# Kernel optimization log

Measured on AMD Instinct MI355X. Metric: run time of the kernel, lower is better.

Reference implementation:

```python
import jax, jax.numpy as jnp
import numpy as np
import math

B, S, D, H, PD = 2, 2048, 1024, 16, 3
DK = D // H          # 64
SP = S // H          # 128, required so physics_scores matches scores shape


def setup_inputs() -> dict:
    key = jax.random.key(0)
    ks = jax.random.split(key, 16)
    sc = 0.02
    return {
        "query": jax.random.normal(ks[0], (B, S, D), jnp.float32),
        "key_in": jax.random.normal(ks[1], (B, S, D), jnp.float32),
        "value": jax.random.normal(ks[2], (B, S, D), jnp.float32),
        "physics_info": jax.random.normal(ks[3], (B, SP, PD), jnp.float32),
        "Wq": jax.random.normal(ks[4], (D, D), jnp.float32) * sc,
        "bq": jnp.zeros((D,), jnp.float32),
        "Wk": jax.random.normal(ks[5], (D, D), jnp.float32) * sc,
        "bk": jnp.zeros((D,), jnp.float32),
        "Wv": jax.random.normal(ks[6], (D, D), jnp.float32) * sc,
        "bv": jnp.zeros((D,), jnp.float32),
        "Wo": jax.random.normal(ks[7], (D, D), jnp.float32) * sc,
        "bo": jnp.zeros((D,), jnp.float32),
        "Pw": jax.random.normal(ks[8], (PD, D), jnp.float32),   # physics_weight
        "pb": jnp.zeros((1,), jnp.float32),                      # physics_bias
    }


def reference(query, key_in, value, physics_info, Wq, bq, Wk, bk, Wv, bv, Wo, bo, Pw, pb):
    b, s, d = query.shape
    inv = 1.0 / math.sqrt(DK)
    # project and split heads -> [B, H, S, DK]
    Q = (query @ Wq + bq).reshape(b, s, H, DK).transpose(0, 2, 1, 3)
    K = (key_in @ Wk + bk).reshape(b, s, H, DK).transpose(0, 2, 1, 3)
    V = (value @ Wv + bv).reshape(b, s, H, DK).transpose(0, 2, 1, 3)
    scores = jnp.einsum('bhqd,bhkd->bhqk', Q, K) * inv  # [B,H,S,S]
    # physics constraint: [B,SP,D] -> (expand over heads is a no-op) -> [B,SP*H,DK]
    pc = (physics_info @ Pw).reshape(b, SP * H, DK)
    physics_scores = jnp.einsum('bhqd,bkd->bhqk', Q, pc) * inv  # [B,H,S,S]
    scores = scores + pb[0] * physics_scores
    attn = jax.nn.softmax(scores, axis=-1)  # dropout in eval mode (identity)
    ctx = jnp.einsum('bhqk,bhkd->bhqd', attn, V)
    ctx = ctx.transpose(0, 2, 1, 3).reshape(b, s, d)
    return ctx @ Wo + bo
```

## Files before the change

kernel.cpp:

```cpp
#include <hip/hip_runtime.h>
#include <hip/hip_bf16.h>
#include <stdint.h>
#include <math.h>

typedef __bf16 bf16_t;
typedef __attribute__((ext_vector_type(8))) __bf16 bf16x8;
typedef __attribute__((ext_vector_type(4))) __bf16 bf16x4;
typedef __attribute__((ext_vector_type(4))) short short4_t;
typedef __attribute__((ext_vector_type(4))) float f32x4;

#define GLOBAL_AS(p) ((const __attribute__((address_space(1))) void*)(p))
#define LDS_AS(p)    ((__attribute__((address_space(3))) void*)(p))

#define B_ 2
#define S_ 2048
#define D_ 1024
#define H_ 16
#define DK_ 64
#define SP_ 128

#define QSCALE 0.1803368801111144f

static __device__ inline float fast_exp2(float x) {
#if __has_builtin(__builtin_amdgcn_exp2f)
    return __builtin_amdgcn_exp2f(x);
#else
    return __expf(x * 0.6931471805599453f);
#endif
}

static __device__ inline f32x4 mfma16x16x16bf16(short4_t a, short4_t b, f32x4 c) {
#if __has_builtin(__builtin_amdgcn_mfma_f32_16x16x16bf16_1k)
    return __builtin_amdgcn_mfma_f32_16x16x16bf16_1k(a, b, c, 0, 0, 0);
#else
    asm volatile("v_mfma_f32_16x16x16_bf16 %0, %1, %2, %0" : "+v"(c) : "v"(a), "v"(b));
    return c;
#endif
}

struct WPtrs { const float* w[4]; bf16_t* o[4]; };

__global__ __launch_bounds__(256) void prep(
    const float* __restrict__ q, const float* __restrict__ k,
    const float* __restrict__ v,
    bf16_t* __restrict__ qo, bf16_t* __restrict__ ko, bf16_t* __restrict__ vo,
    WPtrs wp, const float* __restrict__ phys, const float* __restrict__ Pw,
    float* __restrict__ PP) {
    __shared__ bf16_t t[32][33];
    int tid = threadIdx.x;
    for (int bx = blockIdx.x; bx < 11264; bx += 2048) {
        if (bx < 6144) {
            int z = bx >> 11, blk = bx & 2047;
            const float* in = (z == 0) ? q : (z == 1) ? k : v;
            bf16_t* out = (z == 0) ? qo : (z == 1) ? ko : vo;
            size_t i = ((size_t)blk * 256 + tid) * 8;
            f32x4 a = *(const f32x4*)(in + i);
            f32x4 b = *(const f32x4*)(in + i + 4);
            bf16x8 o;
#pragma unroll
            for (int e = 0; e < 4; ++e) { o[e] = (bf16_t)a[e]; o[4 + e] = (bf16_t)b[e]; }
            *(bf16x8*)(out + i) = o;
        } else if (bx < 10240) {
            __syncthreads();
            int idx = bx - 6144;
            int z = idx >> 10;
            const float* W = wp.w[z];
            bf16_t* Wt = wp.o[z];
            int gx = (idx & 31) * 32, gy = ((idx >> 5) & 31) * 32;
            int x = tid & 31, y0 = tid >> 5;
#pragma unroll
            for (int j = 0; j < 32; j += 8)
                t[y0 + j][x] = (bf16_t)W[(size_t)(gy + y0 + j) * D_ + gx + x];
            __syncthreads();
#pragma unroll
            for (int j = 0; j < 32; j += 8)
                Wt[(size_t)(gx + y0 + j) * D_ + gy + x] = t[x][y0 + j];
        } else {
            int i = (bx - 10240) * 256 + tid;
            int n = i & (D_ - 1);
            int sb = i >> 10;
            float acc = 0.f;
#pragma unroll
            for (int p = 0; p < 3; ++p)
                acc += phys[sb * 3 + p] * Pw[p * D_ + n];
            PP[i] = acc;
        }
    }
}

#define TSTR 272

__global__ __launch_bounds__(256) void qkv_gemm(
    const bf16_t* __restrict__ Qi, const bf16_t* __restrict__ Ki,
    const bf16_t* __restrict__ Vi,
    const bf16_t* __restrict__ WqT, const bf16_t* __restrict__ WkT,
    const bf16_t* __restrict__ WvT,
    const float* __restrict__ bq, const float* __restrict__ bk,
    const float* __restrict__ bv,
    bf16_t* __restrict__ Qo, bf16_t* __restrict__ Ko, bf16_t* __restrict__ Vo,
    const float* __restrict__ PP, const float* __restrict__ pbp) {
    __shared__ alignas(16) char smem[40960];
    bf16_t* lA = (bf16_t*)smem;
    bf16_t* lB = (bf16_t*)(smem + 16384);
    int z = blockIdx.z;
    const bf16_t* A = (z == 0) ? Qi : (z == 1) ? Ki : Vi;
    const bf16_t* Bt = (z == 0) ? WqT : (z == 1) ? WkT : WvT;
    const float* bias = (z == 0) ? bq : (z == 1) ? bk : bv;

    int tid = threadIdx.x;
    int lane = tid & 63, wid = tid >> 6;
    int quad = lane >> 4, l15 = lane & 15;
    int bm = blockIdx.x * 128;
    int bn = blockIdx.y * 128;
    int wm = (wid >> 1) * 64, wn = (wid & 1) * 64;
    f32x4 acc[4][4] = {};

    for (int k0 = 0; k0 < D_; k0 += 64) {
        __syncthreads();
        const char* gA = (const char*)(A + (size_t)bm * D_ + k0);
        const char* gB = (const char*)(Bt + (size_t)bn * D_ + k0);
#pragma unroll
        for (int j = 0; j < 4; ++j) {
            int woff = j * 4096 + wid * 1024;
            int fl = woff + lane * 16;
            int row = fl >> 7, col = fl & 127;
            __builtin_amdgcn_global_load_lds(GLOBAL_AS(gA + (size_t)row * (D_ * 2) + col),
                                             LDS_AS((char*)lA + woff), 16, 0, 0);
            __builtin_amdgcn_global_load_lds(GLOBAL_AS(gB + (size_t)row * (D_ * 2) + col),
                                             LDS_AS((char*)lB + woff), 16, 0, 0);
        }
        __syncthreads();
#pragma unroll
        for (int ks = 0; ks < 2; ++ks) {
            bf16x8 af[4], bfr[4];
#pragma unroll
            for (int i = 0; i < 4; ++i) {
                af[i] = *(const bf16x8*)((const char*)lA + (wm + i * 16 + l15) * 128 + ks * 64 + quad * 16);
                bfr[i] = *(const bf16x8*)((const char*)lB + (wn + i * 16 + l15) * 128 + ks * 64 + quad * 16);
            }
#pragma unroll
            for (int i = 0; i < 4; ++i)
#pragma unroll
                for (int j = 0; j < 4; ++j)
                    acc[i][j] = __builtin_amdgcn_mfma_f32_16x16x32_bf16(af[i], bfr[j], acc[i][j], 0, 0, 0);
        }
    }

    __syncthreads();
    float pb0 = (z == 1) ? pbp[0] : 0.f;
    char* T = smem;
#pragma unroll
    for (int i = 0; i < 4; ++i)
#pragma unroll
        for (int j = 0; j < 4; ++j) {
            int rl0 = wm + i * 16 + quad * 4;
            int c = wn + j * 16 + l15;
            float bv_ = bias[bn + c];
            if (z == 2) {
                bf16x4 t4;
#pragma unroll
                for (int reg = 0; reg < 4; ++reg) t4[reg] = (bf16_t)(acc[i][j][reg] + bv_);
                *(bf16x4*)(T + c * TSTR + rl0 * 2) = t4;
            } else if (z == 1) {
#pragma unroll
                for (int reg = 0; reg < 4; ++reg) {
                    int r = bm + rl0 + reg;
                    int b = r >> 11, s = r & (S_ - 1);
                    float v = acc[i][j][reg] + bv_ +
                              pb0 * PP[((size_t)(b * SP_ + (s >> 4)) << 10) + ((s & 15) << 6) + ((bn + c) & 63)];
                    *(bf16_t*)(T + (rl0 + reg) * TSTR + c * 2) = (bf16_t)v;
                }
            } else {
#pragma unroll
                for (int reg = 0; reg < 4; ++reg)
                    *(bf16_t*)(T + (rl0 + reg) * TSTR + c * 2) = (bf16_t)((acc[i][j][reg] + bv_) * QSCALE);
            }
        }
    __syncthreads();
    if (z == 2) {
        int b = bm >> 11, s0 = bm & (S_ - 1);
        char* gout = (char*)Vo + (((size_t)(b << 10) + bn) * S_ + s0) * 2;
#pragma unroll
        for (int it = 0; it < 8; ++it) {
            int chunk = it * 256 + tid;
            int row = chunk >> 4, c16 = chunk & 15;
            bf16x8 v = *(const bf16x8*)(T + row * TSTR + c16 * 16);
            *(bf16x8*)(gout + (size_t)row * (S_ * 2) + c16 * 16) = v;
        }
    } else {
        bf16_t* O = (z == 0) ? Qo : Ko;
        char* gout = (char*)(O + (size_t)bm * D_ + bn);
#pragma unroll
        for (int it = 0; it < 8; ++it) {
            int chunk = it * 256 + tid;
            int row = chunk >> 4, c16 = chunk & 15;
            bf16x8 v = *(const bf16x8*)(T + row * TSTR + c16 * 16);
            *(bf16x8*)(gout + (size_t)row * (D_ * 2) + c16 * 16) = v;
        }
    }
}

#define KSTR 144
#define VSTR 272

__global__ __launch_bounds__(256) void flash_attn(const bf16_t* Qb,
                                                  const bf16_t* __restrict__ Kb,
                                                  const bf16_t* __restrict__ Vt,
                                                  bf16_t* Ctx) {
    __shared__ alignas(16) char lK[128 * KSTR];
    __shared__ alignas(16) char lV[64 * VSTR];
    int tid = threadIdx.x, lane = tid & 63, wid = tid >> 6;
    int quad = lane >> 4, l15 = lane & 15;
    int q0 = blockIdx.x * 128;
    int h = blockIdx.y, b = blockIdx.z;
    const bf16_t* Qh = Qb + ((size_t)b * S_) * D_ + h * DK_;
    const bf16_t* Kh = Kb + ((size_t)b * S_) * D_ + h * DK_;
    const bf16_t* Vh = Vt + ((size_t)b * D_ + h * DK_) * S_;

    {
        const char* g = (const char*)(Qh + (size_t)q0 * D_);
#pragma unroll
        for (int j = 0; j < 4; ++j) {
            int flat = j * 4096 + tid * 16;
            bf16x8 v = *(const bf16x8*)(g + (size_t)(flat >> 7) * (D_ * 2) + (flat & 127));
            *(bf16x8*)(lK + (flat >> 7) * KSTR + (flat & 127)) = v;
        }
    }
    __syncthreads();
    bf16x8 qf[2][2];
#pragma unroll
    for (int mt = 0; mt < 2; ++mt)
#pragma unroll
        for (int ks = 0; ks < 2; ++ks)
            qf[mt][ks] = *(const bf16x8*)(lK + (wid * 32 + mt * 16 + l15) * KSTR + ks * 64 + quad * 16);

    f32x4 ot[4][2] = {};
    float l_i[2] = {0.f, 0.f};

    for (int t = 0; t < S_ / 128; ++t) {
        const char* gK = (const char*)(Kh + (size_t)t * 128 * D_);
        const char* gV = (const char*)(Vh + (size_t)t * 128);
        bf16x8 vk[4], vv[4];
#pragma unroll
        for (int j = 0; j < 4; ++j) {
            int flat = j * 4096 + tid * 16;
            vk[j] = *(const bf16x8*)(gK + (size_t)(flat >> 7) * (D_ * 2) + (flat & 127));
            vv[j] = *(const bf16x8*)(gV + (size_t)(flat >> 8) * (S_ * 2) + (flat & 255));
        }
        __syncthreads();
#pragma unroll
        for (int j = 0; j < 4; ++j) {
            int flat = j * 4096 + tid * 16;
            *(bf16x8*)(lK + (flat >> 7) * KSTR + (flat & 127)) = vk[j];
            *(bf16x8*)(lV + (flat >> 8) * VSTR + (flat & 255)) = vv[j];
        }
        __syncthreads();

        f32x4 sc[8][2];
#pragma unroll
        for (int kt = 0; kt < 8; ++kt)
#pragma unroll
            for (int mt = 0; mt < 2; ++mt) sc[kt][mt] = (f32x4){0.f, 0.f, 0.f, 0.f};
#pragma unroll
        for (int kt = 0; kt < 8; ++kt) {
            bf16x8 kf0 = *(const bf16x8*)(lK + (kt * 16 + l15) * KSTR + quad * 16);
            bf16x8 kf1 = *(const bf16x8*)(lK + (kt * 16 + l15) * KSTR + 64 + quad * 16);
#pragma unroll
            for (int mt = 0; mt < 2; ++mt) {
                sc[kt][mt] = __builtin_amdgcn_mfma_f32_16x16x32_bf16(kf0, qf[mt][0], sc[kt][mt], 0, 0, 0);
                sc[kt][mt] = __builtin_amdgcn_mfma_f32_16x16x32_bf16(kf1, qf[mt][1], sc[kt][mt], 0, 0, 0);
            }
        }

#pragma unroll
        for (int mt = 0; mt < 2; ++mt) {
            float rsum = 0.f;
#pragma unroll
            for (int kt = 0; kt < 8; ++kt)
#pragma unroll
                for (int r = 0; r < 4; ++r) {
                    float p = fast_exp2(sc[kt][mt][r]);
                    sc[kt][mt][r] = p;
                    rsum += p;
                }
            rsum += __shfl_xor(rsum, 16, 64);
            rsum += __shfl_xor(rsum, 32, 64);
            l_i[mt] += rsum;
        }

#pragma unroll
        for (int kt = 0; kt < 8; ++kt) {
            short4_t bp[2];
#pragma unroll
            for (int mt = 0; mt < 2; ++mt) {
                bf16x4 t4;
#pragma unroll
                for (int r = 0; r < 4; ++r) t4[r] = (bf16_t)sc[kt][mt][r];
                bp[mt] = *(short4_t*)&t4;
            }
#pragma unroll
            for (int dt = 0; dt < 4; ++dt) {
                bf16x4 a4 = *(const bf16x4*)(lV + (dt * 16 + l15) * VSTR + kt * 32 + quad * 8);
                short4_t ap = *(short4_t*)&a4;
#pragma unroll
                for (int mt = 0; mt < 2; ++mt)
                    ot[dt][mt] = mfma16x16x16bf16(ap, bp[mt], ot[dt][mt]);
            }
        }
    }

    __syncthreads();
#pragma unroll
    for (int mt = 0; mt < 2; ++mt) {
        float inv_l = 1.0f / l_i[mt];
#pragma unroll
        for (int dt = 0; dt < 4; ++dt) {
            bf16x4 t4;
#pragma unroll
            for (int r = 0; r < 4; ++r) t4[r] = (bf16_t)(ot[dt][mt][r] * inv_l);
            *(bf16x4*)(lK + (wid * 32 + mt * 16 + l15) * KSTR + dt * 32 + quad * 8) = t4;
        }
    }
    __syncthreads();
    {
        char* gout = (char*)(Ctx + ((size_t)b * S_ + q0) * D_ + h * DK_);
#pragma unroll
        for (int j = 0; j < 4; ++j) {
            int flat = j * 4096 + tid * 16;
            bf16x8 v = *(const bf16x8*)(lK + (flat >> 7) * KSTR + (flat & 127));
            *(bf16x8*)(gout + (size_t)(flat >> 7) * (D_ * 2) + (flat & 127)) = v;
        }
    }
}

__global__ __launch_bounds__(256) void gemm_out(const bf16_t* __restrict__ A,
                                                const bf16_t* __restrict__ Bt,
                                                const float* __restrict__ bias,
                                                float* __restrict__ C) {
    __shared__ alignas(16) bf16_t lA[64 * 64];
    __shared__ alignas(16) bf16_t lB[128 * 64];
    int tid = threadIdx.x;
    int lane = tid & 63, wid = tid >> 6;
    int quad = lane >> 4, l15 = lane & 15;
    int bm = blockIdx.x * 64;
    int bn = blockIdx.y * 128;
    int wm = (wid >> 1) * 32, wn = (wid & 1) * 64;
    f32x4 acc[2][4] = {};

    for (int k0 = 0; k0 < D_; k0 += 64) {
        __syncthreads();
        const char* gA = (const char*)(A + (size_t)bm * D_ + k0);
        const char* gB = (const char*)(Bt + (size_t)bn * D_ + k0);
#pragma unroll
        for (int j = 0; j < 2; ++j) {
            int fl = j * 4096 + tid * 16;
            int row = fl >> 7, col = fl & 127;
            __builtin_amdgcn_global_load_lds(GLOBAL_AS(gA + (size_t)row * (D_ * 2) + col),
                                             LDS_AS((char*)lA + fl), 16, 0, 0);
        }
#pragma unroll
        for (int j = 0; j < 4; ++j) {
            int fl = j * 4096 + tid * 16;
            int row = fl >> 7, col = fl & 127;
            __builtin_amdgcn_global_load_lds(GLOBAL_AS(gB + (size_t)row * (D_ * 2) + col),
                                             LDS_AS((char*)lB + fl), 16, 0, 0);
        }
        __syncthreads();
#pragma unroll
        for (int ks = 0; ks < 2; ++ks) {
            bf16x8 af[2], bfr[4];
#pragma unroll
            for (int i = 0; i < 2; ++i)
                af[i] = *(const bf16x8*)((const char*)lA + (wm + i * 16 + l15) * 128 + ks * 64 + quad * 16);
#pragma unroll
            for (int j = 0; j < 4; ++j)
                bfr[j] = *(const bf16x8*)((const char*)lB + (wn + j * 16 + l15) * 128 + ks * 64 + quad * 16);
#pragma unroll
            for (int i = 0; i < 2; ++i)
#pragma unroll
                for (int j = 0; j < 4; ++j)
                    acc[i][j] = __builtin_amdgcn_mfma_f32_16x16x32_bf16(af[i], bfr[j], acc[i][j], 0, 0, 0);
        }
    }
#pragma unroll
    for (int i = 0; i < 2; ++i)
#pragma unroll
        for (int j = 0; j < 4; ++j) {
            int r0 = bm + wm + i * 16 + quad * 4;
            int c = bn + wn + j * 16 + l15;
            float bv_ = bias[c];
#pragma unroll
            for (int reg = 0; reg < 4; ++reg)
                C[(size_t)(r0 + reg) * D_ + c] = acc[i][j][reg] + bv_;
        }
}

extern "C" void kernel_launch(void* const* d_in, const int* in_sizes, int n_in,
                              void* d_out, int out_size, void* d_ws, size_t ws_size,
                              hipStream_t stream) {
    const float* query  = (const float*)d_in[0];
    const float* key_in = (const float*)d_in[1];
    const float* value  = (const float*)d_in[2];
    const float* phys   = (const float*)d_in[3];
    const float* Wq     = (const float*)d_in[4];
    const float* bq     = (const float*)d_in[5];
    const float* Wk     = (const float*)d_in[6];
    const float* bk     = (const float*)d_in[7];
    const float* Wv     = (const float*)d_in[8];
    const float* bv     = (const float*)d_in[9];
    const float* Wo     = (const float*)d_in[10];
    const float* bo     = (const float*)d_in[11];
    const float* Pw     = (const float*)d_in[12];
    const float* pb     = (const float*)d_in[13];

    char* ws = (char*)d_ws;
    const size_t MB = 1ull << 20;
    bf16_t* Kb  = (bf16_t*)(ws + 0 * MB);
    bf16_t* QC  = (bf16_t*)(ws + 8 * MB);
    bf16_t* Kin = (bf16_t*)(ws + 16 * MB);
    bf16_t* Vin = (bf16_t*)(ws + 24 * MB);
    bf16_t* WqT = (bf16_t*)(ws + 32 * MB);
    bf16_t* WkT = (bf16_t*)(ws + 34 * MB);
    bf16_t* WvT = (bf16_t*)(ws + 36 * MB);
    bf16_t* WoT = (bf16_t*)(ws + 38 * MB);
    float*  PP  = (float*)(ws + 40 * MB);
    bf16_t* Vt  = (bf16_t*)d_out;
    bf16_t* Qin = (bf16_t*)((char*)d_out + 8 * MB);

    WPtrs wp;
    wp.w[0] = Wq; wp.w[1] = Wk; wp.w[2] = Wv; wp.w[3] = Wo;
    wp.o[0] = WqT; wp.o[1] = WkT; wp.o[2] = WvT; wp.o[3] = WoT;

    prep<<<2048, 256, 0, stream>>>(query, key_in, value, Qin, Kin, Vin,
                                   wp, phys, Pw, PP);

    dim3 gq(32, 8, 3);
    qkv_gemm<<<gq, 256, 0, stream>>>(Qin, Kin, Vin, WqT, WkT, WvT,
                                     bq, bk, bv, QC, Kb, Vt, PP, pb);

    dim3 fg(S_ / 128, H_, B_);
    flash_attn<<<fg, 256, 0, stream>>>(QC, Kb, Vt, QC);

    dim3 gg(64, 8);
    gemm_out<<<gg, 256, 0, stream>>>(QC, WoT, bo, (float*)d_out);
}
```

Measured before the change: 247.5 us.

## Make flash attention wave-independent with async double-buffered LDS loads

Each wave now owns 32 query rows of a (batch, head) pair and streams K/V tiles of 32 keys into its own private LDS buffers. It uses global_load_lds with double buffering and explicit vmcnt waits, which removes all block-level __syncthreads. K rows are XOR-swizzled to avoid bank conflicts, and Q fragments are read straight from global memory. Output is written directly without staging through LDS. Each wave now issues 64 small iterations, so per-iteration overhead grows, the four waves of a block fetch no shared K/V, and 64KB of LDS per block may limit occupancy.

```diff
diff --git a/kernel.cpp b/kernel.cpp
--- a/kernel.cpp
+++ b/kernel.cpp
@@ -200,83 +200,108 @@
     }
 }
 
-#define KSTR 144
-#define VSTR 272
-
 __global__ __launch_bounds__(256) void flash_attn(const bf16_t* Qb,
                                                   const bf16_t* __restrict__ Kb,
                                                   const bf16_t* __restrict__ Vt,
                                                   bf16_t* Ctx) {
-    __shared__ alignas(16) char lK[128 * KSTR];
-    __shared__ alignas(16) char lV[64 * VSTR];
+    __shared__ alignas(16) char lds[65536];
     int tid = threadIdx.x, lane = tid & 63, wid = tid >> 6;
     int quad = lane >> 4, l15 = lane & 15;
-    int q0 = blockIdx.x * 128;
-    int h = blockIdx.y, b = blockIdx.z;
-    const bf16_t* Qh = Qb + ((size_t)b * S_) * D_ + h * DK_;
-    const bf16_t* Kh = Kb + ((size_t)b * S_) * D_ + h * DK_;
-    const bf16_t* Vh = Vt + ((size_t)b * D_ + h * DK_) * S_;
-
-    {
-        const char* g = (const char*)(Qh + (size_t)q0 * D_);
-#pragma unroll
-        for (int j = 0; j < 4; ++j) {
-            int flat = j * 4096 + tid * 16;
-            bf16x8 v = *(const bf16x8*)(g + (size_t)(flat >> 7) * (D_ * 2) + (flat & 127));
-            *(bf16x8*)(lK + (flat >> 7) * KSTR + (flat & 127)) = v;
-        }
-    }
-    __syncthreads();
+    char* wK = lds + wid * 16384;
+    char* wV = wK + 8192;
+
+    int gw = blockIdx.x * 4 + wid;
+    int bh = gw >> 6;
+    int q0 = (gw & 63) * 32;
+    int h = bh & 15, b = bh >> 4;
+
+    const char* Qh = (const char*)(Qb + ((size_t)b * S_) * D_ + h * DK_);
+    const char* Kh = (const char*)(Kb + ((size_t)b * S_) * D_ + h * DK_);
+    const char* Vh = (const char*)(Vt + ((size_t)(b << 10) + h * DK_) * S_);
+
     bf16x8 qf[2][2];
 #pragma unroll
     for (int mt = 0; mt < 2; ++mt)
 #pragma unroll
         for (int ks = 0; ks < 2; ++ks)
-            qf[mt][ks] = *(const bf16x8*)(lK + (wid * 32 + mt * 16 + l15) * KSTR + ks * 64 + quad * 16);
+            qf[mt][ks] = *(const bf16x8*)(Qh + (size_t)(q0 + mt * 16 + l15) * (D_ * 2) +
+                                          ks * 64 + quad * 16);
+
+    auto STAGE = [&](int t) {
+        char* dK = wK + (t & 1) * 4096;
+        char* dV = wV + (t & 1) * 4096;
+        const char* sK = Kh + (size_t)(t * 32) * (D_ * 2);
+        const char* sV = Vh + t * 64;
+#pragma unroll
+        for (int l = 0; l < 4; ++l) {
+            int f = l * 1024 + lane * 16;
+            int row = f >> 7, c2 = f & 127;
+            __builtin_amdgcn_global_load_lds(
+                GLOBAL_AS(sK + (size_t)row * (D_ * 2) + (c2 ^ ((row & 7) << 4))),
+                LDS_AS(dK + l * 1024), 16, 0, 0);
+        }
+#pragma unroll
+        for (int l = 0; l < 4; ++l) {
+            int f = l * 1024 + lane * 16;
+            int row = f >> 6, c2 = f & 63;
+            __builtin_amdgcn_global_load_lds(
+                GLOBAL_AS(sV + (size_t)row * (S_ * 2) + c2),
+                LDS_AS(dV + l * 1024), 16, 0, 0);
+        }
+    };
 
     f32x4 ot[4][2] = {};
     float l_i[2] = {0.f, 0.f};
 
-    for (int t = 0; t < S_ / 128; ++t) {
-        const char* gK = (const char*)(Kh + (size_t)t * 128 * D_);
-        const char* gV = (const char*)(Vh + (size_t)t * 128);
-        bf16x8 vk[4], vv[4];
-#pragma unroll
-        for (int j = 0; j < 4; ++j) {
-            int flat = j * 4096 + tid * 16;
-            vk[j] = *(const bf16x8*)(gK + (size_t)(flat >> 7) * (D_ * 2) + (flat & 127));
-            vv[j] = *(const bf16x8*)(gV + (size_t)(flat >> 8) * (S_ * 2) + (flat & 255));
-        }
-        __syncthreads();
-#pragma unroll
-        for (int j = 0; j < 4; ++j) {
-            int flat = j * 4096 + tid * 16;
-            *(bf16x8*)(lK + (flat >> 7) * KSTR + (flat & 127)) = vk[j];
-            *(bf16x8*)(lV + (flat >> 8) * VSTR + (flat & 255)) = vv[j];
-        }
-        __syncthreads();
-
-        f32x4 sc[8][2];
-#pragma unroll
-        for (int kt = 0; kt < 8; ++kt)
+    STAGE(0);
+    STAGE(1);
+
+    for (int t = 0; t < 64; ++t) {
+        if (t < 63) asm volatile("s_waitcnt vmcnt(8)" ::: "memory");
+        else        asm volatile("s_waitcnt vmcnt(0)" ::: "memory");
+        __builtin_amdgcn_sched_barrier(0);
+
+        const char* bK = wK + (t & 1) * 4096;
+        const char* bV = wV + (t & 1) * 4096;
+
+        bf16x8 kf[2][2];
+#pragma unroll
+        for (int kt = 0; kt < 2; ++kt)
+#pragma unroll
+            for (int ks = 0; ks < 2; ++ks)
+                kf[kt][ks] = *(const bf16x8*)(bK + (kt * 16 + l15) * 128 +
+                                              ((ks * 64 + quad * 16) ^ ((l15 & 7) << 4)));
+        bf16x4 vf[2][4];
+#pragma unroll
+        for (int kt = 0; kt < 2; ++kt)
+#pragma unroll
+            for (int dt = 0; dt < 4; ++dt)
+                vf[kt][dt] = *(const bf16x4*)(bV + (dt * 16 + l15) * 64 + kt * 32 + quad * 8);
+        asm volatile("s_waitcnt lgkmcnt(0)" ::: "memory");
+        __builtin_amdgcn_sched_barrier(0);
+
+        if (t < 62) STAGE(t + 2);
+
+        f32x4 sc[2][2];
+#pragma unroll
+        for (int kt = 0; kt < 2; ++kt)
 #pragma unroll
             for (int mt = 0; mt < 2; ++mt) sc[kt][mt] = (f32x4){0.f, 0.f, 0.f, 0.f};
-#pragma unroll
-        for (int kt = 0; kt < 8; ++kt) {
-            bf16x8 kf0 = *(const bf16x8*)(lK + (kt * 16 + l15) * KSTR + quad * 16);
-            bf16x8 kf1 = *(const bf16x8*)(lK + (kt * 16 + l15) * KSTR + 64 + quad * 16);
+        __builtin_amdgcn_s_setprio(1);
+#pragma unroll
+        for (int kt = 0; kt < 2; ++kt)
 #pragma unroll
             for (int mt = 0; mt < 2; ++mt) {
-                sc[kt][mt] = __builtin_amdgcn_mfma_f32_16x16x32_bf16(kf0, qf[mt][0], sc[kt][mt], 0, 0, 0);
-                sc[kt][mt] = __builtin_amdgcn_mfma_f32_16x16x32_bf16(kf1, qf[mt][1], sc[kt][mt], 0, 0, 0);
+                sc[kt][mt] = __builtin_amdgcn_mfma_f32_16x16x32_bf16(kf[kt][0], qf[mt][0], sc[kt][mt], 0, 0, 0);
+                sc[kt][mt] = __builtin_amdgcn_mfma_f32_16x16x32_bf16(kf[kt][1], qf[mt][1], sc[kt][mt], 0, 0, 0);
             }
-        }
+        __builtin_amdgcn_s_setprio(0);
 
 #pragma unroll
         for (int mt = 0; mt < 2; ++mt) {
             float rsum = 0.f;
 #pragma unroll
-            for (int kt = 0; kt < 8; ++kt)
+            for (int kt = 0; kt < 2; ++kt)
 #pragma unroll
                 for (int r = 0; r < 4; ++r) {
                     float p = fast_exp2(sc[kt][mt][r]);
@@ -288,8 +313,9 @@
             l_i[mt] += rsum;
         }
 
-#pragma unroll
-        for (int kt = 0; kt < 8; ++kt) {
+        __builtin_amdgcn_s_setprio(1);
+#pragma unroll
+        for (int kt = 0; kt < 2; ++kt) {
             short4_t bp[2];
 #pragma unroll
             for (int mt = 0; mt < 2; ++mt) {
@@ -300,35 +326,25 @@
             }
 #pragma unroll
             for (int dt = 0; dt < 4; ++dt) {
-                bf16x4 a4 = *(const bf16x4*)(lV + (dt * 16 + l15) * VSTR + kt * 32 + quad * 8);
-                short4_t ap = *(short4_t*)&a4;
+                short4_t ap = *(short4_t*)&vf[kt][dt];
 #pragma unroll
                 for (int mt = 0; mt < 2; ++mt)
                     ot[dt][mt] = mfma16x16x16bf16(ap, bp[mt], ot[dt][mt]);
             }
         }
-    }
-
-    __syncthreads();
+        __builtin_amdgcn_s_setprio(0);
+    }
+
 #pragma unroll
     for (int mt = 0; mt < 2; ++mt) {
         float inv_l = 1.0f / l_i[mt];
+        char* orow = (char*)Ctx + ((size_t)(b * S_ + q0 + mt * 16 + l15) * D_ + h * DK_) * 2;
 #pragma unroll
         for (int dt = 0; dt < 4; ++dt) {
             bf16x4 t4;
 #pragma unroll
             for (int r = 0; r < 4; ++r) t4[r] = (bf16_t)(ot[dt][mt][r] * inv_l);
-            *(bf16x4*)(lK + (wid * 32 + mt * 16 + l15) * KSTR + dt * 32 + quad * 8) = t4;
-        }
-    }
-    __syncthreads();
-    {
-        char* gout = (char*)(Ctx + ((size_t)b * S_ + q0) * D_ + h * DK_);
-#pragma unroll
-        for (int j = 0; j < 4; ++j) {
-            int flat = j * 4096 + tid * 16;
-            bf16x8 v = *(const bf16x8*)(lK + (flat >> 7) * KSTR + (flat & 127));
-            *(bf16x8*)(gout + (size_t)(flat >> 7) * (D_ * 2) + (flat & 127)) = v;
+            *(bf16x4*)(orow + dt * 32 + quad * 8) = t4;
         }
     }
 }
@@ -438,8 +454,7 @@
     qkv_gemm<<<gq, 256, 0, stream>>>(Qin, Kin, Vin, WqT, WkT, WvT,
                                      bq, bk, bv, QC, Kb, Vt, PP, pb);
 
-    dim3 fg(S_ / 128, H_, B_);
-    flash_attn<<<fg, 256, 0, stream>>>(QC, Kb, Vt, QC);
+    flash_attn<<<512, 256, 0, stream>>>(QC, Kb, Vt, QC);
 
     dim3 gg(64, 8);
     gemm_out<<<gg, 256, 0, stream>>>(QC, WoT, bo, (float*)d_out);
```

Measured after the change: 281.0 us. 1.14x slower.
